# Performance work log

Measured on AMD Instinct MI355X. Metric: run time of the kernel, lower is better.

The kernel has to match this reference:

```python
import jax, jax.numpy as jnp
import numpy as np

N_NODES = 100000
N_EDGES = 1600000

def _graph_conv(x, src, dst, W_rel, b_rel, W_root):
    # sum-aggregate source features at destination nodes (PyG GraphConv, aggr='add')
    agg = jax.ops.segment_sum(x[src], dst, num_segments=N_NODES)  # [N, Fin]
    return agg @ W_rel.T + b_rel + x @ W_root.T  # [N, Fout]

def setup_inputs() -> dict:
    key = jax.random.key(0)
    ks = jax.random.split(key, 10)
    x = jax.random.normal(ks[0], (N_NODES, 4), dtype=jnp.float32)
    edge_index = jax.random.randint(ks[1], (2, N_EDGES), 0, N_NODES, dtype=jnp.int32)
    def lin(k, fo, fi):
        return jax.random.normal(k, (fo, fi), dtype=jnp.float32) / np.sqrt(fi)
    return {
        "x": x,
        "edge_index": edge_index,
        "W1_rel": lin(ks[2], 128, 4),
        "b1": jax.random.normal(ks[3], (128,), dtype=jnp.float32) * 0.01,
        "W1_root": lin(ks[4], 128, 4),
        "W2_rel": lin(ks[5], 128, 128),
        "b2": jax.random.normal(ks[6], (128,), dtype=jnp.float32) * 0.01,
        "W2_root": lin(ks[7], 128, 128),
        "Wlin": lin(ks[8], 2, 128),
        "blin": jax.random.normal(ks[9], (2,), dtype=jnp.float32) * 0.01,
    }

def reference(x, edge_index, W1_rel, b1, W1_root, W2_rel, b2, W2_root, Wlin, blin):
    src, dst = edge_index[0], edge_index[1]
    h = jax.nn.relu(_graph_conv(x, src, dst, W1_rel, b1, W1_root))   # [N,128]
    h = jax.nn.relu(_graph_conv(h, src, dst, W2_rel, b2, W2_root))   # [N,128]
    # global_mean_pool with batch = zeros -> mean over all nodes, single graph
    g = jnp.mean(h, axis=0, keepdims=True)                           # [1,128]
    return g @ Wlin.T + blin                                         # [1,2]
```

## Files before the change

### kernel.cpp

```cpp
#include <hip/hip_runtime.h>
#include <cstddef>

#define N_NODES 100000
#define N_EDGES 1600000
#define NCHUNK32 3125
#define GEMM_BLOCKS ((NCHUNK32 + 3) / 4)
#define BUCK_SHIFT 6
#define BUCK_NODES 64
#define NBUCK 1563
#define EB_CAP 1536
#define BF_EDGES 8192
#define BF_BLOCKS ((N_EDGES + BF_EDGES - 1) / BF_EDGES)

typedef __attribute__((ext_vector_type(8))) short short8;
typedef __attribute__((ext_vector_type(4))) float f32x4;
typedef __attribute__((ext_vector_type(2))) float f32x2;

__device__ __forceinline__ unsigned pack_bf16x2(float a, float b) {
  unsigned ua = __float_as_uint(a); ua += 0x7FFFu + ((ua >> 16) & 1u);
  unsigned ub = __float_as_uint(b); ub += 0x7FFFu + ((ub >> 16) & 1u);
  return (ua >> 16) | (ub & 0xFFFF0000u);
}

__global__ __launch_bounds__(512) void k_init(int* __restrict__ bucket_cursor,
                                              float* __restrict__ gsum,
                                              const float* __restrict__ W2_rel,
                                              const float* __restrict__ W2_root,
                                              unsigned* __restrict__ wbuf) {
  int t = threadIdx.x;
  for (int b = t; b < NBUCK; b += 512) bucket_cursor[b] = b * EB_CAP;
  if (t < 128) gsum[t] = 0.0f;
#pragma unroll
  for (int i = 0; i < 8; ++i) {
    int e = t + i * 512;
    int L = e & 63, T = (e >> 6) & 7, K0 = e >> 9;
    int f = T * 16 + (L & 15);
    int k0 = K0 * 32 + ((L >> 4) << 3);
    const float* wsrc = (k0 < 128) ? (W2_rel + f * 128 + k0)
                                   : (W2_root + f * 128 + (k0 - 128));
    float4 w0 = *(const float4*)(wsrc);
    float4 w1 = *(const float4*)(wsrc + 4);
    unsigned* d = wbuf + e * 4;
    d[0] = pack_bf16x2(w0.x, w0.y);
    d[1] = pack_bf16x2(w0.z, w0.w);
    d[2] = pack_bf16x2(w1.x, w1.y);
    d[3] = pack_bf16x2(w1.z, w1.w);
  }
}

__global__ __launch_bounds__(512) void k_bfill(const int* __restrict__ src,
                                               const int* __restrict__ dst,
                                               int* __restrict__ bucket_cursor,
                                               unsigned* __restrict__ ebuf) {
  __shared__ int lh[NBUCK];
  __shared__ int sub_base[NBUCK];
  __shared__ int cur[NBUCK];
  int t = threadIdx.x;
  for (int b = t; b < NBUCK; b += 512) { lh[b] = 0; cur[b] = 0; }
  __syncthreads();
  int e0 = blockIdx.x * BF_EDGES;
  unsigned pk[16];
  int bk[16];
#pragma unroll
  for (int i = 0; i < 16; ++i) {
    int e = e0 + i * 512 + t;
    bk[i] = -1;
    if (e < N_EDGES) {
      int d = dst[e];
      int b = d >> BUCK_SHIFT;
      bk[i] = b;
      pk[i] = ((unsigned)(d & (BUCK_NODES - 1)) << 17) | (unsigned)src[e];
      atomicAdd(&lh[b], 1);
    }
  }
  __syncthreads();
  for (int b = t; b < NBUCK; b += 512)
    sub_base[b] = (lh[b] > 0) ? atomicAdd(&bucket_cursor[b], lh[b]) : 0;
  __syncthreads();
#pragma unroll
  for (int i = 0; i < 16; ++i) {
    if (bk[i] >= 0) {
      int pos = sub_base[bk[i]] + atomicAdd(&cur[bk[i]], 1);
      if (pos < (bk[i] + 1) * EB_CAP) ebuf[pos] = pk[i];
    }
  }
}

__global__ __launch_bounds__(256) void k_fill2(
    const unsigned* __restrict__ ebuf, const int* __restrict__ bucket_cursor,
    const float* __restrict__ x, const float* __restrict__ W1_rel,
    const float* __restrict__ b1, const float* __restrict__ W1_root,
    int* __restrict__ row_start, int* __restrict__ row_end,
    int* __restrict__ csr_src, unsigned short* __restrict__ h1f8) {
  __shared__ int cnt[BUCK_NODES];
  __shared__ int start[BUCK_NODES];
  __shared__ float sagg[BUCK_NODES * 4];
  __shared__ float sx[BUCK_NODES * 4];
  __shared__ float sWa[8 * 128];
  __shared__ float sb1[128];
  int t = threadIdx.x;
  int b = blockIdx.x;
  int base = b * EB_CAP;
  int nb = bucket_cursor[b] - base;
  if (nb > EB_CAP) nb = EB_CAP;
  int n0 = b << BUCK_SHIFT;

  if (t < 128) {
    float4 wr = *(const float4*)(W1_rel + t * 4);
    float4 wo = *(const float4*)(W1_root + t * 4);
    sWa[0 * 128 + t] = wr.x; sWa[1 * 128 + t] = wr.y;
    sWa[2 * 128 + t] = wr.z; sWa[3 * 128 + t] = wr.w;
    sWa[4 * 128 + t] = wo.x; sWa[5 * 128 + t] = wo.y;
    sWa[6 * 128 + t] = wo.z; sWa[7 * 128 + t] = wo.w;
    sb1[t] = b1[t];
  }
  if (t < BUCK_NODES) {
    cnt[t] = 0;
    float4 xv = make_float4(0.f, 0.f, 0.f, 0.f);
    if (n0 + t < N_NODES) xv = *(const float4*)(x + (size_t)(n0 + t) * 4);
    *(float4*)&sx[t * 4] = xv;
  }
  __syncthreads();

  for (int i = t; i < nb; i += 256) atomicAdd(&cnt[ebuf[base + i] >> 17], 1);
  __syncthreads();
  if (t < 64) {
    int v = cnt[t];
    int incl = v;
#pragma unroll
    for (int off = 1; off < 64; off <<= 1) {
      int nvv = __shfl_up(incl, off);
      if (t >= off) incl += nvv;
    }
    int excl = incl - v;
    start[t] = excl;
    cnt[t] = excl;
    if (n0 + t < N_NODES) row_start[n0 + t] = base + excl;
  }
  __syncthreads();
  for (int i = t; i < nb; i += 256) {
    unsigned e = ebuf[base + i];
    int p = atomicAdd(&cnt[e >> 17], 1);
    csr_src[base + p] = (int)(e & 0x1FFFFu);
  }
  __syncthreads();
  {
    int nd = t >> 2, sub = t & 3;
    int rs = base + start[nd];
    int re = base + cnt[nd];
    float4 acc = make_float4(0.f, 0.f, 0.f, 0.f);
    for (int i = rs + sub; i < re; i += 4) {
      int s = csr_src[i];
      float4 v = *(const float4*)(x + (size_t)s * 4);
      acc.x += v.x; acc.y += v.y; acc.z += v.z; acc.w += v.w;
    }
#pragma unroll
    for (int off = 1; off < 4; off <<= 1) {
      acc.x += __shfl_xor(acc.x, off);
      acc.y += __shfl_xor(acc.y, off);
      acc.z += __shfl_xor(acc.z, off);
      acc.w += __shfl_xor(acc.w, off);
    }
    if (sub == 0) *(float4*)&sagg[nd * 4] = acc;
    if (t < 64 && n0 + t < N_NODES) row_end[n0 + t] = base + cnt[t];
  }
  __syncthreads();

  for (int it = t; it < BUCK_NODES * 64; it += 256) {
    int nd = it >> 6;
    if (n0 + nd >= N_NODES) break;
    int fp = it & 63;
    int f = fp * 2;
    float4 a  = *(float4*)&sagg[nd * 4];
    float4 xv = *(float4*)&sx[nd * 4];
    float v0 = sb1[f]
        + a.x  * sWa[0 * 128 + f] + a.y  * sWa[1 * 128 + f]
        + a.z  * sWa[2 * 128 + f] + a.w  * sWa[3 * 128 + f]
        + xv.x * sWa[4 * 128 + f] + xv.y * sWa[5 * 128 + f]
        + xv.z * sWa[6 * 128 + f] + xv.w * sWa[7 * 128 + f];
    int f1 = f + 1;
    float v1 = sb1[f1]
        + a.x  * sWa[0 * 128 + f1] + a.y  * sWa[1 * 128 + f1]
        + a.z  * sWa[2 * 128 + f1] + a.w  * sWa[3 * 128 + f1]
        + xv.x * sWa[4 * 128 + f1] + xv.y * sWa[5 * 128 + f1]
        + xv.z * sWa[6 * 128 + f1] + xv.w * sWa[7 * 128 + f1];
    float r0 = fmaxf(v0, 0.f), r1 = fmaxf(v1, 0.f);
    h1f8[(size_t)(n0 + nd) * 64 + fp] =
        (unsigned short)__builtin_amdgcn_cvt_pk_fp8_f32(r0, r1, 0, false);
  }
}

__global__ __launch_bounds__(256) void k_pull128(
    const unsigned* __restrict__ h1f8_u, const int* __restrict__ row_start,
    const int* __restrict__ row_end, const int* __restrict__ csr_src,
    uint2* __restrict__ agg2b) {
  int w = (blockIdx.x * 256 + threadIdx.x) >> 6;
  if (w >= N_NODES) return;
  int lane = threadIdx.x & 63;
  int half = lane >> 5;
  int hl = lane & 31;
  int rs = row_start[w], re = row_end[w];
  float a0 = 0.f, a1 = 0.f, a2 = 0.f, a3 = 0.f;
  for (int chunk = rs; chunk < re; chunk += 64) {
    int nv = min(64, re - chunk);
    int sv = (chunk + lane < re) ? csr_src[chunk + lane] : 0;
    int j = 0;
    for (; j + 8 <= nv; j += 8) {
      int s0 = __shfl(sv, j + 0 + half);
      int s1 = __shfl(sv, j + 2 + half);
      int s2 = __shfl(sv, j + 4 + half);
      int s3 = __shfl(sv, j + 6 + half);
      unsigned u0 = h1f8_u[(size_t)s0 * 32 + hl];
      unsigned u1 = h1f8_u[(size_t)s1 * 32 + hl];
      unsigned u2 = h1f8_u[(size_t)s2 * 32 + hl];
      unsigned u3 = h1f8_u[(size_t)s3 * 32 + hl];
      f32x2 l0 = __builtin_amdgcn_cvt_pk_f32_fp8((int)u0, false);
      f32x2 h0 = __builtin_amdgcn_cvt_pk_f32_fp8((int)u0, true);
      f32x2 l1 = __builtin_amdgcn_cvt_pk_f32_fp8((int)u1, false);
      f32x2 h1 = __builtin_amdgcn_cvt_pk_f32_fp8((int)u1, true);
      f32x2 l2 = __builtin_amdgcn_cvt_pk_f32_fp8((int)u2, false);
      f32x2 h2 = __builtin_amdgcn_cvt_pk_f32_fp8((int)u2, true);
      f32x2 l3 = __builtin_amdgcn_cvt_pk_f32_fp8((int)u3, false);
      f32x2 h3 = __builtin_amdgcn_cvt_pk_f32_fp8((int)u3, true);
      a0 += l0.x + l1.x + l2.x + l3.x;
      a1 += l0.y + l1.y + l2.y + l3.y;
      a2 += h0.x + h1.x + h2.x + h3.x;
      a3 += h0.y + h1.y + h2.y + h3.y;
    }
    for (; j + 2 <= nv; j += 2) {
      int s0 = __shfl(sv, j + half);
      unsigned u0 = h1f8_u[(size_t)s0 * 32 + hl];
      f32x2 l0 = __builtin_amdgcn_cvt_pk_f32_fp8((int)u0, false);
      f32x2 h0 = __builtin_amdgcn_cvt_pk_f32_fp8((int)u0, true);
      a0 += l0.x; a1 += l0.y; a2 += h0.x; a3 += h0.y;
    }
    if (j < nv) {
      int s0 = __shfl(sv, j);
      unsigned u0 = h1f8_u[(size_t)s0 * 32 + hl];
      if (half == 0) {
        f32x2 l0 = __builtin_amdgcn_cvt_pk_f32_fp8((int)u0, false);
        f32x2 h0 = __builtin_amdgcn_cvt_pk_f32_fp8((int)u0, true);
        a0 += l0.x; a1 += l0.y; a2 += h0.x; a3 += h0.y;
      }
    }
  }
  a0 += __shfl_xor(a0, 32);
  a1 += __shfl_xor(a1, 32);
  a2 += __shfl_xor(a2, 32);
  a3 += __shfl_xor(a3, 32);
  if (half == 0) {
    uint2 o;
    o.x = pack_bf16x2(a0, a1);
    o.y = pack_bf16x2(a2, a3);
    agg2b[(size_t)w * 32 + hl] = o;
  }
}

__global__ __launch_bounds__(256) void k_gemm_pool(
    const unsigned* __restrict__ agg2b_u, const unsigned short* __restrict__ h1f8,
    const unsigned* __restrict__ wbuf_u, const float* __restrict__ b2,
    float* __restrict__ gsum) {
  __shared__ float lgs[128];
  int t = threadIdx.x;
  if (t < 128) lgs[t] = 0.0f;
  __syncthreads();

  int lane = t & 63;
  int gw = blockIdx.x * 4 + (t >> 6);
  int lrow = lane & 15;
  int quad = lane >> 4;
  const unsigned short* agg2b = (const unsigned short*)agg2b_u;
  const unsigned char* h8 = (const unsigned char*)h1f8;
  const short8* wb = (const short8*)wbuf_u;

  float bias[8];
#pragma unroll
  for (int tt = 0; tt < 8; ++tt) bias[tt] = b2[tt * 16 + lrow];
  float csum[8] = {0.f, 0.f, 0.f, 0.f, 0.f, 0.f, 0.f, 0.f};

  if (gw < NCHUNK32) {
    int mbase = gw * 32;

    f32x4 acc[2][8];
#pragma unroll
    for (int mt = 0; mt < 2; ++mt)
#pragma unroll
      for (int tt = 0; tt < 8; ++tt) acc[mt][tt] = (f32x4){0.f, 0.f, 0.f, 0.f};

#pragma unroll
    for (int ks = 0; ks < 4; ++ks) {
      const unsigned short* abase = agg2b + ks * 32 + quad * 8;
      short8 afr[2];
#pragma unroll
      for (int mt = 0; mt < 2; ++mt)
        afr[mt] = *(const short8*)(abase + (size_t)(mbase + mt * 16 + lrow) * 128);
      short8 bfr[8];
#pragma unroll
      for (int tt = 0; tt < 8; ++tt) bfr[tt] = wb[(ks * 8 + tt) * 64 + lane];
#pragma unroll
      for (int mt = 0; mt < 2; ++mt)
#pragma unroll
        for (int tt = 0; tt < 8; ++tt)
          acc[mt][tt] = __builtin_amdgcn_mfma_f32_16x16x32_bf16(
              afr[mt], bfr[tt], acc[mt][tt], 0, 0, 0);
    }
#pragma unroll
    for (int ks = 4; ks < 8; ++ks) {
      short8 afr[2];
#pragma unroll
      for (int mt = 0; mt < 2; ++mt) {
        const uint2* ap = (const uint2*)(h8 + (size_t)(mbase + mt * 16 + lrow) * 128
                                         + (ks - 4) * 32 + quad * 8);
        uint2 u = *ap;
        f32x2 a0 = __builtin_amdgcn_cvt_pk_f32_fp8((int)u.x, false);
        f32x2 a1 = __builtin_amdgcn_cvt_pk_f32_fp8((int)u.x, true);
        f32x2 a2 = __builtin_amdgcn_cvt_pk_f32_fp8((int)u.y, false);
        f32x2 a3 = __builtin_amdgcn_cvt_pk_f32_fp8((int)u.y, true);
        unsigned q[4] = {pack_bf16x2(a0.x, a0.y), pack_bf16x2(a1.x, a1.y),
                         pack_bf16x2(a2.x, a2.y), pack_bf16x2(a3.x, a3.y)};
        afr[mt] = *(short8*)q;
      }
      short8 bfr[8];
#pragma unroll
      for (int tt = 0; tt < 8; ++tt) bfr[tt] = wb[(ks * 8 + tt) * 64 + lane];
#pragma unroll
      for (int mt = 0; mt < 2; ++mt)
#pragma unroll
        for (int tt = 0; tt < 8; ++tt)
          acc[mt][tt] = __builtin_amdgcn_mfma_f32_16x16x32_bf16(
              afr[mt], bfr[tt], acc[mt][tt], 0, 0, 0);
    }

#pragma unroll
    for (int mt = 0; mt < 2; ++mt) {
#pragma unroll
      for (int tt = 0; tt < 8; ++tt) {
        f32x4 v = acc[mt][tt];
        float s = fmaxf(v.x + bias[tt], 0.f) + fmaxf(v.y + bias[tt], 0.f)
                + fmaxf(v.z + bias[tt], 0.f) + fmaxf(v.w + bias[tt], 0.f);
        s += __shfl_xor(s, 16);
        s += __shfl_xor(s, 32);
        csum[tt] += s;
      }
    }
  }
  if (lane < 16) {
#pragma unroll
    for (int tt = 0; tt < 8; ++tt) atomicAdd(&lgs[tt * 16 + lane], csum[tt]);
  }
  __syncthreads();
  if (t < 128) atomicAdd(&gsum[t], lgs[t]);
}

__global__ void k_final(const float* __restrict__ gsum, const float* __restrict__ Wlin,
                        const float* __restrict__ blin, float* __restrict__ out) {
  int lane = threadIdx.x;
  float g0 = gsum[lane];
  float g1 = gsum[lane + 64];
  float s0 = g0 * Wlin[lane]       + g1 * Wlin[lane + 64];
  float s1 = g0 * Wlin[128 + lane] + g1 * Wlin[192 + lane];
#pragma unroll
  for (int off = 32; off > 0; off >>= 1) {
    s0 += __shfl_down(s0, off);
    s1 += __shfl_down(s1, off);
  }
  if (lane == 0) {
    const float inv = 1.0f / (float)N_NODES;
    out[0] = s0 * inv + blin[0];
    out[1] = s1 * inv + blin[1];
  }
}

extern "C" void kernel_launch(void* const* d_in, const int* in_sizes, int n_in,
                              void* d_out, int out_size, void* d_ws, size_t ws_size,
                              hipStream_t stream) {
  const float* x       = (const float*)d_in[0];
  const int*   ei      = (const int*)d_in[1];
  const float* W1_rel  = (const float*)d_in[2];
  const float* b1      = (const float*)d_in[3];
  const float* W1_root = (const float*)d_in[4];
  const float* W2_rel  = (const float*)d_in[5];
  const float* b2      = (const float*)d_in[6];
  const float* W2_root = (const float*)d_in[7];
  const float* Wlin    = (const float*)d_in[8];
  const float* blin    = (const float*)d_in[9];
  const int* src = ei;
  const int* dst = ei + N_EDGES;
  float* out = (float*)d_out;

  char* ws = (char*)d_ws;
  int*            row_start     = (int*)(ws);
  int*            row_end       = (int*)(ws + 400000);
  int*            bucket_cursor = (int*)(ws + 800000);
  float*          gsum          = (float*)(ws + 808192);
  unsigned*       wbuf          = (unsigned*)(ws + 808832);
  int*            csr_src       = (int*)(ws + 874368);
  unsigned*       ebuf          = (unsigned*)(ws + 10477440);
  unsigned short* h1f8          = (unsigned short*)(ws + 20080512);
  uint2*          agg2b         = (uint2*)(ws + 32880512);

  k_init <<<1, 512, 0, stream>>>(bucket_cursor, gsum, W2_rel, W2_root, wbuf);
  k_bfill<<<BF_BLOCKS, 512, 0, stream>>>(src, dst, bucket_cursor, ebuf);
  k_fill2<<<NBUCK, 256, 0, stream>>>(ebuf, bucket_cursor, x, W1_rel, b1, W1_root,
                                     row_start, row_end, csr_src, h1f8);
  k_pull128<<<(N_NODES * 64 + 255) / 256, 256, 0, stream>>>(
      (const unsigned*)h1f8, row_start, row_end, csr_src, agg2b);
  k_gemm_pool<<<GEMM_BLOCKS, 256, 0, stream>>>(
      (const unsigned*)agg2b, h1f8, wbuf, b2, gsum);
  k_final<<<1, 64, 0, stream>>>(gsum, Wlin, blin, out);
}
```

Baseline: 204.3 us.

## Process two nodes per wavefront in pull gather and vectorize edge loads

The pull kernel now has each wavefront aggregate two destination nodes, interleaving their gather loads so more independent memory requests are in flight per wave. Row start and end are packed into one int2 array, so each node needs a single load. The bucket-fill kernel reads src and dst as int4 vectors instead of scalar loads. Launching half as many waves lowers occupancy, and load imbalance between the two paired nodes may leave one tail loop running alone.

```diff
diff --git a/kernel.cpp b/kernel.cpp
--- a/kernel.cpp
+++ b/kernel.cpp
@@ -62,15 +62,32 @@
   unsigned pk[16];
   int bk[16];
 #pragma unroll
-  for (int i = 0; i < 16; ++i) {
-    int e = e0 + i * 512 + t;
-    bk[i] = -1;
-    if (e < N_EDGES) {
-      int d = dst[e];
-      int b = d >> BUCK_SHIFT;
-      bk[i] = b;
-      pk[i] = ((unsigned)(d & (BUCK_NODES - 1)) << 17) | (unsigned)src[e];
-      atomicAdd(&lh[b], 1);
+  for (int i = 0; i < 4; ++i) {
+    int e = e0 + (i * 512 + t) * 4;
+    if (e + 4 <= N_EDGES) {
+      int4 s4 = *(const int4*)(src + e);
+      int4 d4 = *(const int4*)(dst + e);
+      int dd[4] = {d4.x, d4.y, d4.z, d4.w};
+      int ss[4] = {s4.x, s4.y, s4.z, s4.w};
+#pragma unroll
+      for (int j = 0; j < 4; ++j) {
+        int b = dd[j] >> BUCK_SHIFT;
+        bk[i * 4 + j] = b;
+        pk[i * 4 + j] = ((unsigned)(dd[j] & (BUCK_NODES - 1)) << 17) | (unsigned)ss[j];
+        atomicAdd(&lh[b], 1);
+      }
+    } else {
+#pragma unroll
+      for (int j = 0; j < 4; ++j) {
+        bk[i * 4 + j] = -1;
+        if (e + j < N_EDGES) {
+          int d = dst[e + j];
+          int b = d >> BUCK_SHIFT;
+          bk[i * 4 + j] = b;
+          pk[i * 4 + j] = ((unsigned)(d & (BUCK_NODES - 1)) << 17) | (unsigned)src[e + j];
+          atomicAdd(&lh[b], 1);
+        }
+      }
     }
   }
   __syncthreads();
@@ -90,8 +107,8 @@
     const unsigned* __restrict__ ebuf, const int* __restrict__ bucket_cursor,
     const float* __restrict__ x, const float* __restrict__ W1_rel,
     const float* __restrict__ b1, const float* __restrict__ W1_root,
-    int* __restrict__ row_start, int* __restrict__ row_end,
-    int* __restrict__ csr_src, unsigned short* __restrict__ h1f8) {
+    int2* __restrict__ row_se, int* __restrict__ csr_src,
+    unsigned short* __restrict__ h1f8) {
   __shared__ int cnt[BUCK_NODES];
   __shared__ int start[BUCK_NODES];
   __shared__ float sagg[BUCK_NODES * 4];
@@ -135,7 +152,6 @@
     int excl = incl - v;
     start[t] = excl;
     cnt[t] = excl;
-    if (n0 + t < N_NODES) row_start[n0 + t] = base + excl;
   }
   __syncthreads();
   for (int i = t; i < nb; i += 256) {
@@ -162,7 +178,8 @@
       acc.w += __shfl_xor(acc.w, off);
     }
     if (sub == 0) *(float4*)&sagg[nd * 4] = acc;
-    if (t < 64 && n0 + t < N_NODES) row_end[n0 + t] = base + cnt[t];
+    if (t < 64 && n0 + t < N_NODES)
+      row_se[n0 + t] = make_int2(base + start[t], base + cnt[t]);
   }
   __syncthreads();
 
@@ -190,69 +207,146 @@
   }
 }
 
+__device__ __forceinline__ void gather_chunk(
+    const unsigned* __restrict__ h, const int* __restrict__ csr,
+    int chunk, int re, int lane, int half, int hl,
+    float& a0, float& a1, float& a2, float& a3) {
+  int nv = min(64, re - chunk);
+  int sv = (chunk + lane < re) ? csr[chunk + lane] : 0;
+  int j = 0;
+  for (; j + 2 <= nv; j += 2) {
+    int s0 = __shfl(sv, j + half);
+    unsigned u0 = h[(size_t)s0 * 32 + hl];
+    f32x2 l0 = __builtin_amdgcn_cvt_pk_f32_fp8((int)u0, false);
+    f32x2 h0 = __builtin_amdgcn_cvt_pk_f32_fp8((int)u0, true);
+    a0 += l0.x; a1 += l0.y; a2 += h0.x; a3 += h0.y;
+  }
+  if (j < nv) {
+    int s0 = __shfl(sv, j);
+    unsigned u0 = h[(size_t)s0 * 32 + hl];
+    if (half == 0) {
+      f32x2 l0 = __builtin_amdgcn_cvt_pk_f32_fp8((int)u0, false);
+      f32x2 h0 = __builtin_amdgcn_cvt_pk_f32_fp8((int)u0, true);
+      a0 += l0.x; a1 += l0.y; a2 += h0.x; a3 += h0.y;
+    }
+  }
+}
+
 __global__ __launch_bounds__(256) void k_pull128(
-    const unsigned* __restrict__ h1f8_u, const int* __restrict__ row_start,
-    const int* __restrict__ row_end, const int* __restrict__ csr_src,
-    uint2* __restrict__ agg2b) {
-  int w = (blockIdx.x * 256 + threadIdx.x) >> 6;
-  if (w >= N_NODES) return;
+    const unsigned* __restrict__ h1f8_u, const int2* __restrict__ row_se,
+    const int* __restrict__ csr_src, uint2* __restrict__ agg2b) {
+  int gw = (blockIdx.x * 256 + threadIdx.x) >> 6;
+  int w0 = gw * 2;
+  if (w0 >= N_NODES) return;
+  int w1 = w0 + 1;
   int lane = threadIdx.x & 63;
   int half = lane >> 5;
   int hl = lane & 31;
-  int rs = row_start[w], re = row_end[w];
+  int2 se0 = row_se[w0];
+  int2 se1 = row_se[w1];
+  int nv0 = min(64, se0.y - se0.x);
+  int nv1 = min(64, se1.y - se1.x);
+  int sv0 = (se0.x + lane < se0.y) ? csr_src[se0.x + lane] : 0;
+  int sv1 = (se1.x + lane < se1.y) ? csr_src[se1.x + lane] : 0;
   float a0 = 0.f, a1 = 0.f, a2 = 0.f, a3 = 0.f;
-  for (int chunk = rs; chunk < re; chunk += 64) {
-    int nv = min(64, re - chunk);
-    int sv = (chunk + lane < re) ? csr_src[chunk + lane] : 0;
-    int j = 0;
-    for (; j + 8 <= nv; j += 8) {
-      int s0 = __shfl(sv, j + 0 + half);
-      int s1 = __shfl(sv, j + 2 + half);
-      int s2 = __shfl(sv, j + 4 + half);
-      int s3 = __shfl(sv, j + 6 + half);
-      unsigned u0 = h1f8_u[(size_t)s0 * 32 + hl];
-      unsigned u1 = h1f8_u[(size_t)s1 * 32 + hl];
-      unsigned u2 = h1f8_u[(size_t)s2 * 32 + hl];
-      unsigned u3 = h1f8_u[(size_t)s3 * 32 + hl];
-      f32x2 l0 = __builtin_amdgcn_cvt_pk_f32_fp8((int)u0, false);
-      f32x2 h0 = __builtin_amdgcn_cvt_pk_f32_fp8((int)u0, true);
-      f32x2 l1 = __builtin_amdgcn_cvt_pk_f32_fp8((int)u1, false);
-      f32x2 h1 = __builtin_amdgcn_cvt_pk_f32_fp8((int)u1, true);
-      f32x2 l2 = __builtin_amdgcn_cvt_pk_f32_fp8((int)u2, false);
-      f32x2 h2 = __builtin_amdgcn_cvt_pk_f32_fp8((int)u2, true);
-      f32x2 l3 = __builtin_amdgcn_cvt_pk_f32_fp8((int)u3, false);
-      f32x2 h3 = __builtin_amdgcn_cvt_pk_f32_fp8((int)u3, true);
-      a0 += l0.x + l1.x + l2.x + l3.x;
-      a1 += l0.y + l1.y + l2.y + l3.y;
-      a2 += h0.x + h1.x + h2.x + h3.x;
-      a3 += h0.y + h1.y + h2.y + h3.y;
-    }
-    for (; j + 2 <= nv; j += 2) {
-      int s0 = __shfl(sv, j + half);
-      unsigned u0 = h1f8_u[(size_t)s0 * 32 + hl];
+  float c0 = 0.f, c1 = 0.f, c2 = 0.f, c3 = 0.f;
+  int j0 = 0, j1 = 0;
+  while (j0 + 8 <= nv0 && j1 + 8 <= nv1) {
+    int s00 = __shfl(sv0, j0 + 0 + half);
+    int s01 = __shfl(sv0, j0 + 2 + half);
+    int s02 = __shfl(sv0, j0 + 4 + half);
+    int s03 = __shfl(sv0, j0 + 6 + half);
+    int s10 = __shfl(sv1, j1 + 0 + half);
+    int s11 = __shfl(sv1, j1 + 2 + half);
+    int s12 = __shfl(sv1, j1 + 4 + half);
+    int s13 = __shfl(sv1, j1 + 6 + half);
+    unsigned u00 = h1f8_u[(size_t)s00 * 32 + hl];
+    unsigned u01 = h1f8_u[(size_t)s01 * 32 + hl];
+    unsigned u02 = h1f8_u[(size_t)s02 * 32 + hl];
+    unsigned u03 = h1f8_u[(size_t)s03 * 32 + hl];
+    unsigned u10 = h1f8_u[(size_t)s10 * 32 + hl];
+    unsigned u11 = h1f8_u[(size_t)s11 * 32 + hl];
+    unsigned u12 = h1f8_u[(size_t)s12 * 32 + hl];
+    unsigned u13 = h1f8_u[(size_t)s13 * 32 + hl];
+    f32x2 l00 = __builtin_amdgcn_cvt_pk_f32_fp8((int)u00, false);
+    f32x2 h00 = __builtin_amdgcn_cvt_pk_f32_fp8((int)u00, true);
+    f32x2 l01 = __builtin_amdgcn_cvt_pk_f32_fp8((int)u01, false);
+    f32x2 h01 = __builtin_amdgcn_cvt_pk_f32_fp8((int)u01, true);
+    f32x2 l02 = __builtin_amdgcn_cvt_pk_f32_fp8((int)u02, false);
+    f32x2 h02 = __builtin_amdgcn_cvt_pk_f32_fp8((int)u02, true);
+    f32x2 l03 = __builtin_amdgcn_cvt_pk_f32_fp8((int)u03, false);
+    f32x2 h03 = __builtin_amdgcn_cvt_pk_f32_fp8((int)u03, true);
+    a0 += l00.x + l01.x + l02.x + l03.x;
+    a1 += l00.y + l01.y + l02.y + l03.y;
+    a2 += h00.x + h01.x + h02.x + h03.x;
+    a3 += h00.y + h01.y + h02.y + h03.y;
+    f32x2 l10 = __builtin_amdgcn_cvt_pk_f32_fp8((int)u10, false);
+    f32x2 h10 = __builtin_amdgcn_cvt_pk_f32_fp8((int)u10, true);
+    f32x2 l11 = __builtin_amdgcn_cvt_pk_f32_fp8((int)u11, false);
+    f32x2 h11 = __builtin_amdgcn_cvt_pk_f32_fp8((int)u11, true);
+    f32x2 l12 = __builtin_amdgcn_cvt_pk_f32_fp8((int)u12, false);
+    f32x2 h12 = __builtin_amdgcn_cvt_pk_f32_fp8((int)u12, true);
+    f32x2 l13 = __builtin_amdgcn_cvt_pk_f32_fp8((int)u13, false);
+    f32x2 h13 = __builtin_amdgcn_cvt_pk_f32_fp8((int)u13, true);
+    c0 += l10.x + l11.x + l12.x + l13.x;
+    c1 += l10.y + l11.y + l12.y + l13.y;
+    c2 += h10.x + h11.x + h12.x + h13.x;
+    c3 += h10.y + h11.y + h12.y + h13.y;
+    j0 += 8; j1 += 8;
+  }
+  for (; j0 + 2 <= nv0; j0 += 2) {
+    int s0 = __shfl(sv0, j0 + half);
+    unsigned u0 = h1f8_u[(size_t)s0 * 32 + hl];
+    f32x2 l0 = __builtin_amdgcn_cvt_pk_f32_fp8((int)u0, false);
+    f32x2 h0 = __builtin_amdgcn_cvt_pk_f32_fp8((int)u0, true);
+    a0 += l0.x; a1 += l0.y; a2 += h0.x; a3 += h0.y;
+  }
+  if (j0 < nv0) {
+    int s0 = __shfl(sv0, j0);
+    unsigned u0 = h1f8_u[(size_t)s0 * 32 + hl];
+    if (half == 0) {
       f32x2 l0 = __builtin_amdgcn_cvt_pk_f32_fp8((int)u0, false);
       f32x2 h0 = __builtin_amdgcn_cvt_pk_f32_fp8((int)u0, true);
       a0 += l0.x; a1 += l0.y; a2 += h0.x; a3 += h0.y;
     }
-    if (j < nv) {
-      int s0 = __shfl(sv, j);
-      unsigned u0 = h1f8_u[(size_t)s0 * 32 + hl];
-      if (half == 0) {
-        f32x2 l0 = __builtin_amdgcn_cvt_pk_f32_fp8((int)u0, false);
-        f32x2 h0 = __builtin_amdgcn_cvt_pk_f32_fp8((int)u0, true);
-        a0 += l0.x; a1 += l0.y; a2 += h0.x; a3 += h0.y;
-      }
-    }
-  }
+  }
+  for (; j1 + 2 <= nv1; j1 += 2) {
+    int s0 = __shfl(sv1, j1 + half);
+    unsigned u0 = h1f8_u[(size_t)s0 * 32 + hl];
+    f32x2 l0 = __builtin_amdgcn_cvt_pk_f32_fp8((int)u0, false);
+    f32x2 h0 = __builtin_amdgcn_cvt_pk_f32_fp8((int)u0, true);
+    c0 += l0.x; c1 += l0.y; c2 += h0.x; c3 += h0.y;
+  }
+  if (j1 < nv1) {
+    int s0 = __shfl(sv1, j1);
+    unsigned u0 = h1f8_u[(size_t)s0 * 32 + hl];
+    if (half == 0) {
+      f32x2 l0 = __builtin_amdgcn_cvt_pk_f32_fp8((int)u0, false);
+      f32x2 h0 = __builtin_amdgcn_cvt_pk_f32_fp8((int)u0, true);
+      c0 += l0.x; c1 += l0.y; c2 += h0.x; c3 += h0.y;
+    }
+  }
+  for (int chunk = se0.x + 64; chunk < se0.y; chunk += 64)
+    gather_chunk(h1f8_u, csr_src, chunk, se0.y, lane, half, hl, a0, a1, a2, a3);
+  for (int chunk = se1.x + 64; chunk < se1.y; chunk += 64)
+    gather_chunk(h1f8_u, csr_src, chunk, se1.y, lane, half, hl, c0, c1, c2, c3);
+
   a0 += __shfl_xor(a0, 32);
   a1 += __shfl_xor(a1, 32);
   a2 += __shfl_xor(a2, 32);
   a3 += __shfl_xor(a3, 32);
+  c0 += __shfl_xor(c0, 32);
+  c1 += __shfl_xor(c1, 32);
+  c2 += __shfl_xor(c2, 32);
+  c3 += __shfl_xor(c3, 32);
   if (half == 0) {
-    uint2 o;
-    o.x = pack_bf16x2(a0, a1);
-    o.y = pack_bf16x2(a2, a3);
-    agg2b[(size_t)w * 32 + hl] = o;
+    uint2 o0, o1;
+    o0.x = pack_bf16x2(a0, a1);
+    o0.y = pack_bf16x2(a2, a3);
+    o1.x = pack_bf16x2(c0, c1);
+    o1.y = pack_bf16x2(c2, c3);
+    agg2b[(size_t)w0 * 32 + hl] = o0;
+    agg2b[(size_t)w1 * 32 + hl] = o1;
   }
 }
 
@@ -389,8 +483,7 @@
   float* out = (float*)d_out;
 
   char* ws = (char*)d_ws;
-  int*            row_start     = (int*)(ws);
-  int*            row_end       = (int*)(ws + 400000);
+  int2*           row_se        = (int2*)(ws);
   int*            bucket_cursor = (int*)(ws + 800000);
   float*          gsum          = (float*)(ws + 808192);
   unsigned*       wbuf          = (unsigned*)(ws + 808832);
@@ -402,9 +495,9 @@
   k_init <<<1, 512, 0, stream>>>(bucket_cursor, gsum, W2_rel, W2_root, wbuf);
   k_bfill<<<BF_BLOCKS, 512, 0, stream>>>(src, dst, bucket_cursor, ebuf);
   k_fill2<<<NBUCK, 256, 0, stream>>>(ebuf, bucket_cursor, x, W1_rel, b1, W1_root,
-                                     row_start, row_end, csr_src, h1f8);
-  k_pull128<<<(N_NODES * 64 + 255) / 256, 256, 0, stream>>>(
-      (const unsigned*)h1f8, row_start, row_end, csr_src, agg2b);
+                                     row_se, csr_src, h1f8);
+  k_pull128<<<(N_NODES / 2 * 64 + 255) / 256, 256, 0, stream>>>(
+      (const unsigned*)h1f8, row_se, csr_src, agg2b);
   k_gemm_pool<<<GEMM_BLOCKS, 256, 0, stream>>>(
       (const unsigned*)agg2b, h1f8, wbuf, b2, gsum);
   k_final<<<1, 64, 0, stream>>>(gsum, Wlin, blin, out);
```

New measurement: 201.0 us, median of 2. No clear change (-1.6%).
